# Kernel tuning notes

Measured on AMD Instinct MI355X. Metric: run time of the kernel, lower is better.

The kernel has to match this reference:

```python
import jax, jax.numpy as jnp
import numpy as np

N_RES = 700
D = 1024
HIDDEN = 1024
OUT = 1


def setup_inputs() -> dict:
    key = jax.random.key(0)
    k1, k2, k3 = jax.random.split(key, 3)
    B = 128
    s_s = jax.random.normal(k1, (N_RES, B, D), dtype=jnp.float32)
    # MLP params: hidden Linear(1024->1024) + ReLU, then Linear(1024->out)
    W1 = jax.random.normal(k2, (D, HIDDEN), dtype=jnp.float32) * (1.0 / np.sqrt(D))
    b1 = jnp.zeros((HIDDEN,), dtype=jnp.float32)
    W2 = jax.random.normal(k3, (HIDDEN, OUT), dtype=jnp.float32) * (1.0 / np.sqrt(HIDDEN))
    b2 = jnp.zeros((OUT,), dtype=jnp.float32)
    return {"s_s": s_s, "W1": W1, "b1": b1, "W2": W2, "b2": b2}


def reference(s_s, W1, b1, W2, b2):
    # Original loops over 700 residue slices; math is identical to one batched MLP.
    x = s_s.reshape(N_RES, -1, D)                 # [700, B, 1024]
    h = jax.nn.relu(jnp.einsum('rbd,dh->rbh', x, W1) + b1)
    y = jnp.einsum('rbh,ho->rbo', h, W2) + b2     # [700, B, out]
    return jnp.transpose(y, (1, 0, 2))            # stack dim=1 -> [B, 700, out]
```

## Files before the change

kernel.cpp:

```cpp
#include <hip/hip_runtime.h>
#include <hip/hip_bf16.h>

typedef __attribute__((ext_vector_type(8))) short short8;
typedef __attribute__((ext_vector_type(4))) float floatx4;

#define NRES 700
#define DDIM 1024
#define HID 1024

__device__ __forceinline__ unsigned short f2bf(float f) {
  unsigned u = __float_as_uint(f);
  u = (u + 0x7FFFu + ((u >> 16) & 1u)) >> 16;
  return (unsigned short)u;
}

__device__ __forceinline__ void async_copy16(void* lds, const void* g) {
  __builtin_amdgcn_global_load_lds(
      (const __attribute__((address_space(1))) unsigned*)g,
      (__attribute__((address_space(3))) unsigned*)lds, 16, 0, 0);
}

__global__ void convert_a_kernel(const float* __restrict__ A,
                                 unsigned short* __restrict__ Abf, long n8) {
  long i = (long)blockIdx.x * blockDim.x + threadIdx.x;
  long stride = (long)gridDim.x * blockDim.x;
  for (; i < n8; i += stride) {
    const float* p = A + i * 8;
    float4 f0 = *(const float4*)p;
    float4 f1 = *(const float4*)(p + 4);
    int4 pk;
    pk.x = f2bf(f0.x) | ((unsigned)f2bf(f0.y) << 16);
    pk.y = f2bf(f0.z) | ((unsigned)f2bf(f0.w) << 16);
    pk.z = f2bf(f1.x) | ((unsigned)f2bf(f1.y) << 16);
    pk.w = f2bf(f1.z) | ((unsigned)f2bf(f1.w) << 16);
    *(int4*)(Abf + i * 8) = pk;
  }
}

__global__ void transpose_w1_kernel(const float* __restrict__ W1,
                                    unsigned short* __restrict__ W1T) {
  __shared__ float tile[32][33];
  int bx = blockIdx.x, by = blockIdx.y;
  int tx = threadIdx.x, ty = threadIdx.y;
#pragma unroll
  for (int i = 0; i < 32; i += 8)
    tile[ty + i][tx] = W1[(size_t)(by * 32 + ty + i) * HID + bx * 32 + tx];
  __syncthreads();
#pragma unroll
  for (int i = 0; i < 32; i += 8)
    W1T[(size_t)(bx * 32 + ty + i) * DDIM + by * 32 + tx] = f2bf(tile[tx][ty + i]);
}

__global__ void init_out_kernel(float* __restrict__ out, const float* __restrict__ b2, int n) {
  int i = blockIdx.x * blockDim.x + threadIdx.x;
  if (i < n) out[i] = b2[0];
}

__launch_bounds__(256, 2)
__global__ void fused_mlp_kernel(const unsigned short* __restrict__ Abf,
                                 const unsigned short* __restrict__ W1T,
                                 const float* __restrict__ b1,
                                 const float* __restrict__ W2,
                                 float* __restrict__ out) {
  __shared__ __align__(16) unsigned short As[128 * 64];
  __shared__ __align__(16) unsigned short Bs[128 * 64];

  int bid = blockIdx.x;
  int w = (bid & 7) * 700 + (bid >> 3);
  int blk_m = w >> 3;
  int blk_n = w & 7;
  int m0 = blk_m * 128;
  int n0 = blk_n * 128;

  int t = threadIdx.x;
  int lane = t & 63;
  int wid = t >> 6;
  int wm = wid >> 1, wn = wid & 1;
  int lrow = lane & 15, lk = lane >> 4;

  floatx4 acc[4][4];
#pragma unroll
  for (int i = 0; i < 4; ++i)
#pragma unroll
    for (int j = 0; j < 4; ++j) acc[i][j] = (floatx4)(0.f);

  for (int kt = 0; kt < 16; ++kt) {
    int k0 = kt * 64;
#pragma unroll
    for (int i = 0; i < 4; ++i) {
      int base_chunk = i * 256 + wid * 64;
      int c = base_chunk + lane;
      int row = c >> 3, slot = c & 7;
      int sc = slot ^ (row & 7);
      async_copy16(&As[base_chunk * 8], Abf + (size_t)(m0 + row) * DDIM + k0 + sc * 8);
      async_copy16(&Bs[base_chunk * 8], W1T + (size_t)(n0 + row) * DDIM + k0 + sc * 8);
    }
    __syncthreads();

#pragma unroll
    for (int ks = 0; ks < 2; ++ks) {
      short8 af[4], bf[4];
#pragma unroll
      for (int f = 0; f < 4; ++f) {
        int arow = wm * 64 + f * 16 + lrow;
        int ac = (ks * 4 + lk) ^ (arow & 7);
        af[f] = *(const short8*)(&As[arow * 64 + ac * 8]);
        int brow = wn * 64 + f * 16 + lrow;
        int bc = (ks * 4 + lk) ^ (brow & 7);
        bf[f] = *(const short8*)(&Bs[brow * 64 + bc * 8]);
      }
#pragma unroll
      for (int fm = 0; fm < 4; ++fm)
#pragma unroll
        for (int fn = 0; fn < 4; ++fn)
          acc[fm][fn] = __builtin_amdgcn_mfma_f32_16x16x32_bf16(af[fm], bf[fn], acc[fm][fn], 0, 0, 0);
    }
    __syncthreads();
  }

  float w2v[4], b1v[4];
#pragma unroll
  for (int fn = 0; fn < 4; ++fn) {
    int col = n0 + wn * 64 + fn * 16 + lrow;
    w2v[fn] = W2[col];
    b1v[fn] = b1[col];
  }
#pragma unroll
  for (int fm = 0; fm < 4; ++fm) {
#pragma unroll
    for (int j = 0; j < 4; ++j) {
      float p = 0.f;
#pragma unroll
      for (int fn = 0; fn < 4; ++fn) {
        float h = acc[fm][fn][j] + b1v[fn];
        h = fmaxf(h, 0.f);
        p += h * w2v[fn];
      }
      p += __shfl_xor(p, 1);
      p += __shfl_xor(p, 2);
      p += __shfl_xor(p, 4);
      p += __shfl_xor(p, 8);
      if ((lane & 15) == 0) {
        int row = wm * 64 + fm * 16 + (lk << 2) + j;
        atomicAdd(&out[row * NRES + blk_m], p);
      }
    }
  }
}

__launch_bounds__(256, 2)
__global__ void fused_mlp_fallback(const float* __restrict__ A,
                                   const unsigned short* __restrict__ W1T,
                                   const float* __restrict__ b1,
                                   const float* __restrict__ W2,
                                   float* __restrict__ out) {
  __shared__ unsigned short As[128 * 64];
  __shared__ unsigned short Bs[128 * 64];
  int bid = blockIdx.x;
  int w = (bid & 7) * 700 + (bid >> 3);
  int blk_m = w >> 3, blk_n = w & 7;
  int m0 = blk_m * 128, n0 = blk_n * 128;
  int t = threadIdx.x, lane = t & 63, wid = t >> 6;
  int wm = wid >> 1, wn = wid & 1;
  int lrow = lane & 15, lk = lane >> 4;
  floatx4 acc[4][4];
#pragma unroll
  for (int i = 0; i < 4; ++i)
#pragma unroll
    for (int j = 0; j < 4; ++j) acc[i][j] = (floatx4)(0.f);
  for (int kt = 0; kt < 16; ++kt) {
    int k0 = kt * 64;
#pragma unroll
    for (int i = 0; i < 4; ++i) {
      int c = i * 256 + t;
      int row = c >> 3, c8 = c & 7;
      int dst = row * 64 + ((c8 ^ (row & 7)) * 8);
      const float* gp = A + (size_t)(m0 + row) * DDIM + k0 + c8 * 8;
      float4 f0 = *(const float4*)gp;
      float4 f1 = *(const float4*)(gp + 4);
      int4 pk;
      pk.x = f2bf(f0.x) | ((unsigned)f2bf(f0.y) << 16);
      pk.y = f2bf(f0.z) | ((unsigned)f2bf(f0.w) << 16);
      pk.z = f2bf(f1.x) | ((unsigned)f2bf(f1.y) << 16);
      pk.w = f2bf(f1.z) | ((unsigned)f2bf(f1.w) << 16);
      *(int4*)(&As[dst]) = pk;
      const unsigned short* gb = W1T + (size_t)(n0 + row) * DDIM + k0 + c8 * 8;
      *(int4*)(&Bs[dst]) = *(const int4*)gb;
    }
    __syncthreads();
#pragma unroll
    for (int ks = 0; ks < 2; ++ks) {
      short8 af[4], bf[4];
#pragma unroll
      for (int f = 0; f < 4; ++f) {
        int arow = wm * 64 + f * 16 + lrow;
        int ac = (ks * 4 + lk) ^ (arow & 7);
        af[f] = *(const short8*)(&As[arow * 64 + ac * 8]);
        int brow = wn * 64 + f * 16 + lrow;
        int bc = (ks * 4 + lk) ^ (brow & 7);
        bf[f] = *(const short8*)(&Bs[brow * 64 + bc * 8]);
      }
#pragma unroll
      for (int fm = 0; fm < 4; ++fm)
#pragma unroll
        for (int fn = 0; fn < 4; ++fn)
          acc[fm][fn] = __builtin_amdgcn_mfma_f32_16x16x32_bf16(af[fm], bf[fn], acc[fm][fn], 0, 0, 0);
    }
    __syncthreads();
  }
  float w2v[4], b1v[4];
#pragma unroll
  for (int fn = 0; fn < 4; ++fn) {
    int col = n0 + wn * 64 + fn * 16 + lrow;
    w2v[fn] = W2[col];
    b1v[fn] = b1[col];
  }
#pragma unroll
  for (int fm = 0; fm < 4; ++fm) {
#pragma unroll
    for (int j = 0; j < 4; ++j) {
      float p = 0.f;
#pragma unroll
      for (int fn = 0; fn < 4; ++fn) {
        float h = acc[fm][fn][j] + b1v[fn];
        h = fmaxf(h, 0.f);
        p += h * w2v[fn];
      }
      p += __shfl_xor(p, 1);
      p += __shfl_xor(p, 2);
      p += __shfl_xor(p, 4);
      p += __shfl_xor(p, 8);
      if ((lane & 15) == 0) {
        int row = wm * 64 + fm * 16 + (lk << 2) + j;
        atomicAdd(&out[row * NRES + blk_m], p);
      }
    }
  }
}

extern "C" void kernel_launch(void* const* d_in, const int* in_sizes, int n_in,
                              void* d_out, int out_size, void* d_ws, size_t ws_size,
                              hipStream_t stream) {
  const float* s_s = (const float*)d_in[0];
  const float* W1 = (const float*)d_in[1];
  const float* b1 = (const float*)d_in[2];
  const float* W2 = (const float*)d_in[3];
  const float* b2 = (const float*)d_in[4];
  float* out = (float*)d_out;

  unsigned short* W1T = (unsigned short*)d_ws;
  const size_t w1t_bytes = (size_t)HID * DDIM * 2;
  const size_t abf_bytes = (size_t)NRES * 128 * DDIM * 2;

  dim3 tb(32, 8);
  dim3 tg(HID / 32, DDIM / 32);
  transpose_w1_kernel<<<tg, tb, 0, stream>>>(W1, W1T);

  init_out_kernel<<<(out_size + 255) / 256, 256, 0, stream>>>(out, b2, out_size);

  if (ws_size >= w1t_bytes + abf_bytes) {
    unsigned short* Abf = (unsigned short*)((char*)d_ws + w1t_bytes);
    long n8 = (long)NRES * 128 * DDIM / 8;
    convert_a_kernel<<<2048, 256, 0, stream>>>(s_s, Abf, n8);
    fused_mlp_kernel<<<NRES * 8, 256, 0, stream>>>(Abf, W1T, b1, W2, out);
  } else {
    fused_mlp_fallback<<<NRES * 8, 256, 0, stream>>>(s_s, W1T, b1, W2, out);
  }
}
```

Measured before the change: 302.6 us.

## Use 256x256 tiles with triple-buffered async LDS pipeline in fused MLP GEMM

Replaces the 128x128, single-buffered GEMM with a 512-thread kernel computing 256x256 tiles and a K-step of 32. Loads are triple-buffered and prefetched two steps ahead using vmcnt waits and raw barriers, and MFMA issue priority is raised during compute. The aim is to hide global-load latency and halve redundant A/B traffic per output. In exchange, per-thread accumulators grow to 128 floats, which may pressure registers and occupancy.

```diff
diff --git a/kernel.cpp b/kernel.cpp
--- a/kernel.cpp
+++ b/kernel.cpp
@@ -56,93 +56,115 @@
   if (i < n) out[i] = b2[0];
 }
 
-__launch_bounds__(256, 2)
-__global__ void fused_mlp_kernel(const unsigned short* __restrict__ Abf,
-                                 const unsigned short* __restrict__ W1T,
-                                 const float* __restrict__ b1,
-                                 const float* __restrict__ W2,
-                                 float* __restrict__ out) {
-  __shared__ __align__(16) unsigned short As[128 * 64];
-  __shared__ __align__(16) unsigned short Bs[128 * 64];
+__launch_bounds__(512, 2)
+__global__ void gemm256_kernel(const unsigned short* __restrict__ Abf,
+                               const unsigned short* __restrict__ W1T,
+                               const float* __restrict__ b1,
+                               const float* __restrict__ W2,
+                               float* __restrict__ out) {
+  __shared__ __align__(16) unsigned short As[3][256 * 32];
+  __shared__ __align__(16) unsigned short Bs[3][256 * 32];
 
   int bid = blockIdx.x;
-  int w = (bid & 7) * 700 + (bid >> 3);
-  int blk_m = w >> 3;
-  int blk_n = w & 7;
-  int m0 = blk_m * 128;
-  int n0 = blk_n * 128;
-
-  int t = threadIdx.x;
-  int lane = t & 63;
-  int wid = t >> 6;
-  int wm = wid >> 1, wn = wid & 1;
+  int w = (bid & 7) * 175 + (bid >> 3);
+  int blk_m = w >> 2;
+  int blk_n = w & 3;
+  int m0 = blk_m * 256;
+  int n0 = blk_n * 256;
+
+  int tid = threadIdx.x;
+  int lane = tid & 63;
+  int wid = tid >> 6;
+  int wm = wid >> 2, wn = wid & 3;
   int lrow = lane & 15, lk = lane >> 4;
 
-  floatx4 acc[4][4];
-#pragma unroll
-  for (int i = 0; i < 4; ++i)
+  floatx4 acc[8][4];
+#pragma unroll
+  for (int i = 0; i < 8; ++i)
 #pragma unroll
     for (int j = 0; j < 4; ++j) acc[i][j] = (floatx4)(0.f);
 
-  for (int kt = 0; kt < 16; ++kt) {
-    int k0 = kt * 64;
-#pragma unroll
-    for (int i = 0; i < 4; ++i) {
-      int base_chunk = i * 256 + wid * 64;
-      int c = base_chunk + lane;
-      int row = c >> 3, slot = c & 7;
-      int sc = slot ^ (row & 7);
-      async_copy16(&As[base_chunk * 8], Abf + (size_t)(m0 + row) * DDIM + k0 + sc * 8);
-      async_copy16(&Bs[base_chunk * 8], W1T + (size_t)(n0 + row) * DDIM + k0 + sc * 8);
-    }
-    __syncthreads();
-
-#pragma unroll
-    for (int ks = 0; ks < 2; ++ks) {
-      short8 af[4], bf[4];
-#pragma unroll
-      for (int f = 0; f < 4; ++f) {
-        int arow = wm * 64 + f * 16 + lrow;
-        int ac = (ks * 4 + lk) ^ (arow & 7);
-        af[f] = *(const short8*)(&As[arow * 64 + ac * 8]);
-        int brow = wn * 64 + f * 16 + lrow;
-        int bc = (ks * 4 + lk) ^ (brow & 7);
-        bf[f] = *(const short8*)(&Bs[brow * 64 + bc * 8]);
-      }
-#pragma unroll
-      for (int fm = 0; fm < 4; ++fm)
-#pragma unroll
-        for (int fn = 0; fn < 4; ++fn)
-          acc[fm][fn] = __builtin_amdgcn_mfma_f32_16x16x32_bf16(af[fm], bf[fn], acc[fm][fn], 0, 0, 0);
-    }
-    __syncthreads();
+  auto stage = [&](int t) {
+    int buf = t % 3;
+    int k0 = t * 32;
+#pragma unroll
+    for (int i = 0; i < 2; ++i) {
+      int d = i * 512 + tid;
+      int row = d >> 2, slot = d & 3;
+      int sc = slot ^ (row & 3);
+      int dbase = (d & ~63) * 8;
+      async_copy16(&As[buf][dbase], Abf + (size_t)(m0 + row) * DDIM + k0 + sc * 8);
+      async_copy16(&Bs[buf][dbase], W1T + (size_t)(n0 + row) * DDIM + k0 + sc * 8);
+    }
+  };
+
+  auto compute = [&](int t) {
+    int buf = t % 3;
+    short8 af[8], bfv[4];
+#pragma unroll
+    for (int f = 0; f < 8; ++f) {
+      int row = wm * 128 + f * 16 + lrow;
+      int slot = lk ^ (row & 3);
+      af[f] = *(const short8*)&As[buf][row * 32 + slot * 8];
+    }
+#pragma unroll
+    for (int g = 0; g < 4; ++g) {
+      int row = wn * 64 + g * 16 + lrow;
+      int slot = lk ^ (row & 3);
+      bfv[g] = *(const short8*)&Bs[buf][row * 32 + slot * 8];
+    }
+#pragma unroll
+    for (int f = 0; f < 8; ++f)
+#pragma unroll
+      for (int g = 0; g < 4; ++g)
+        acc[f][g] = __builtin_amdgcn_mfma_f32_16x16x32_bf16(af[f], bfv[g], acc[f][g], 0, 0, 0);
+  };
+
+  stage(0);
+  stage(1);
+  asm volatile("s_waitcnt vmcnt(4)" ::: "memory");
+  __builtin_amdgcn_s_barrier();
+
+  for (int t = 0; t < 32; ++t) {
+    bool pf = (t + 2) < 32;
+    if (pf) stage(t + 2);
+    __builtin_amdgcn_s_setprio(1);
+    compute(t);
+    __builtin_amdgcn_s_setprio(0);
+    if (t + 1 < 32) {
+      if (pf)
+        asm volatile("s_waitcnt vmcnt(4)" ::: "memory");
+      else
+        asm volatile("s_waitcnt vmcnt(0)" ::: "memory");
+      __builtin_amdgcn_s_barrier();
+    }
   }
 
   float w2v[4], b1v[4];
 #pragma unroll
-  for (int fn = 0; fn < 4; ++fn) {
-    int col = n0 + wn * 64 + fn * 16 + lrow;
-    w2v[fn] = W2[col];
-    b1v[fn] = b1[col];
-  }
-#pragma unroll
-  for (int fm = 0; fm < 4; ++fm) {
+  for (int g = 0; g < 4; ++g) {
+    int col = n0 + wn * 64 + g * 16 + lrow;
+    w2v[g] = W2[col];
+    b1v[g] = b1[col];
+  }
+#pragma unroll
+  for (int f = 0; f < 8; ++f) {
 #pragma unroll
     for (int j = 0; j < 4; ++j) {
       float p = 0.f;
 #pragma unroll
-      for (int fn = 0; fn < 4; ++fn) {
-        float h = acc[fm][fn][j] + b1v[fn];
+      for (int g = 0; g < 4; ++g) {
+        float h = acc[f][g][j] + b1v[g];
         h = fmaxf(h, 0.f);
-        p += h * w2v[fn];
+        p += h * w2v[g];
       }
       p += __shfl_xor(p, 1);
       p += __shfl_xor(p, 2);
       p += __shfl_xor(p, 4);
       p += __shfl_xor(p, 8);
       if ((lane & 15) == 0) {
-        int row = wm * 64 + fm * 16 + (lk << 2) + j;
-        atomicAdd(&out[row * NRES + blk_m], p);
+        int grow = m0 + wm * 128 + f * 16 + (lk << 2) + j;
+        atomicAdd(&out[(grow & 127) * NRES + (grow >> 7)], p);
       }
     }
   }
@@ -262,7 +284,7 @@
     unsigned short* Abf = (unsigned short*)((char*)d_ws + w1t_bytes);
     long n8 = (long)NRES * 128 * DDIM / 8;
     convert_a_kernel<<<2048, 256, 0, stream>>>(s_s, Abf, n8);
-    fused_mlp_kernel<<<NRES * 8, 256, 0, stream>>>(Abf, W1T, b1, W2, out);
+    gemm256_kernel<<<350 * 4, 512, 0, stream>>>(Abf, W1T, b1, W2, out);
   } else {
     fused_mlp_fallback<<<NRES * 8, 256, 0, stream>>>(s_s, W1T, b1, W2, out);
   }
```

Result: slower. 421.2 us (+39.2%).
